# Optimization experiments

Measured on AMD Instinct MI355X. Metric: run time of the kernel, lower is better.

The kernel has to match this reference:

```python
import jax, jax.numpy as jnp
import numpy as np

# Dims (match init_kwargs)
B, S, D = 2, 2048, 2048
H = 16
Q_LORA, KV_LORA = 768, 512
NOPE, ROPE, VD = 128, 64, 128
QHD = NOPE + ROPE  # 192


def setup_inputs() -> dict:
    key = jax.random.key(0)
    ks = jax.random.split(key, 7)
    w = lambda k, shape: (jax.random.normal(k, shape, jnp.float32) * 0.02)
    return {
        "x": jax.random.normal(ks[0], (B, S, D), jnp.float32),
        "position": jnp.broadcast_to(jnp.arange(S, dtype=jnp.int32), (B, S)),
        "mask": jnp.tril(jnp.ones((1, 1, S, S), jnp.int32)),  # causal
        "w_q_down": w(ks[1], (D, Q_LORA)),                 # (in, out) layout
        "w_q_up": w(ks[2], (Q_LORA, H * QHD)),
        "w_kv_down": w(ks[3], (D, KV_LORA + ROPE)),
        "w_kv_up": w(ks[4], (KV_LORA, H * (NOPE + VD))),
        "w_out": w(ks[5], (H * VD, D)),
    }


def reference(x, position, mask, w_q_down, w_q_up, w_kv_down, w_kv_up, w_out):
    # position unused: rope_embedding is None in the source module.
    # Low-rank Q: down then up projection.
    q = (x @ w_q_down) @ w_q_up                      # [B,S,H*QHD]
    q = q.reshape(B, S, H, QHD).transpose(0, 2, 1, 3)  # [B,H,S,QHD]
    q_nope, q_rope = q[..., :NOPE], q[..., NOPE:]

    # Low-rank KV: down projection yields compressed kv + shared rope key.
    c = x @ w_kv_down                                # [B,S,KV_LORA+ROPE]
    c_kv, k_rope = c[..., :KV_LORA], c[..., KV_LORA:]
    k_rope = k_rope[:, None, :, :]                   # [B,1,S,ROPE]

    kv = (c_kv @ w_kv_up).reshape(B, S, H, NOPE + VD).transpose(0, 2, 1, 3)
    k_nope, v = kv[..., :NOPE], kv[..., NOPE:]       # [B,H,S,NOPE], [B,H,S,VD]

    q_state = jnp.concatenate([q_nope, q_rope], axis=-1)           # [B,H,S,QHD]
    k_state = jnp.concatenate(
        [k_nope, jnp.broadcast_to(k_rope, (B, H, S, ROPE))], axis=-1)

    scale = 1.0 / jnp.sqrt(jnp.float32(VD))  # source divides by sqrt(v_head_dim)
    scores = jnp.einsum("bhqd,bhkd->bhqk", q_state, k_state) * scale
    scores = jnp.where(mask == 0, jnp.float32(-jnp.inf), scores)
    att = jax.nn.softmax(scores, axis=-1)            # dropout_rate=0 (eval)
    out = jnp.einsum("bhqk,bhkd->bhqd", att, v)      # [B,H,S,VD]
    out = out.transpose(0, 2, 1, 3).reshape(B, S, H * VD)
    return out @ w_out
```

## Files before the change

kernel.cpp:

```cpp
#include <hip/hip_runtime.h>

typedef __bf16 bf16;
typedef bf16 bf16x8 __attribute__((ext_vector_type(8)));
typedef bf16 bf16x4 __attribute__((ext_vector_type(4)));
typedef float f32x4 __attribute__((ext_vector_type(4)));
typedef short s16x4 __attribute__((ext_vector_type(4)));

#define AS1 __attribute__((address_space(1)))
#define AS3 __attribute__((address_space(3)))

__device__ __forceinline__ void load_lds16(const void* g, void* l) {
    __builtin_amdgcn_global_load_lds((const AS1 unsigned int*)g,
                                     (AS3 unsigned int*)l, 16, 0, 0);
}

__global__ __launch_bounds__(256) void cast_f32_bf16(
        const float* __restrict__ in, bf16* __restrict__ out, int n) {
    int i = (blockIdx.x * 256 + threadIdx.x) * 4;
    if (i < n) {
        float4 v = *(const float4*)(in + i);
        bf16x4 o = { (bf16)v.x, (bf16)v.y, (bf16)v.z, (bf16)v.w };
        *(bf16x4*)(out + i) = o;
    }
}

__global__ __launch_bounds__(256) void transpose_cast(
        const float* __restrict__ in, bf16* __restrict__ out,
        int K, int N, int Np) {
    __shared__ float tile[32][33];
    int bx = blockIdx.x * 32;
    int by = blockIdx.y * 32;
    int tx = threadIdx.x, ty = threadIdx.y;
#pragma unroll
    for (int i = 0; i < 4; ++i) {
        int k = by + ty + i * 8, n = bx + tx;
        float v = (k < K && n < N) ? in[(size_t)k * N + n] : 0.f;
        tile[ty + i * 8][tx] = v;
    }
    __syncthreads();
#pragma unroll
    for (int i = 0; i < 4; ++i) {
        int n = bx + ty + i * 8, k = by + tx;
        if (n < Np && k < K) out[(size_t)n * K + k] = (bf16)tile[tx][ty + i * 8];
    }
}

template <typename OutT>
__global__ __launch_bounds__(256) void gemm_bt(
        const bf16* __restrict__ A, const bf16* __restrict__ Bt,
        OutT* __restrict__ C, int K, int lda, int ldb, int ldc) {
    __shared__ __align__(16) bf16 As[128 * 64];
    __shared__ __align__(16) bf16 Bs[128 * 64];
    const int tid = threadIdx.x;
    const int wave = tid >> 6, lane = tid & 63;
    const int l15 = lane & 15, quad = lane >> 4;
    const int m0 = blockIdx.y * 128, n0 = blockIdx.x * 128;
    const int wm = (wave >> 1) * 64, wn = (wave & 1) * 64;

    f32x4 acc[4][4] = {};

    for (int k0 = 0; k0 < K; k0 += 64) {
#pragma unroll
        for (int c = 0; c < 4; ++c) {
            int e = wave * 2048 + c * 512 + lane * 8;
            int r = e >> 6, col = e & 63;
            load_lds16(A + (size_t)(m0 + r) * lda + k0 + col,
                       &As[wave * 2048 + c * 512]);
            load_lds16(Bt + (size_t)(n0 + r) * ldb + k0 + col,
                       &Bs[wave * 2048 + c * 512]);
        }
        __syncthreads();
#pragma unroll
        for (int kk = 0; kk < 64; kk += 32) {
            bf16x8 af[4], bf[4];
#pragma unroll
            for (int i = 0; i < 4; ++i)
                af[i] = *(const bf16x8*)&As[(wm + i * 16 + l15) * 64 + kk + quad * 8];
#pragma unroll
            for (int j = 0; j < 4; ++j)
                bf[j] = *(const bf16x8*)&Bs[(wn + j * 16 + l15) * 64 + kk + quad * 8];
#pragma unroll
            for (int i = 0; i < 4; ++i)
#pragma unroll
                for (int j = 0; j < 4; ++j)
                    acc[i][j] = __builtin_amdgcn_mfma_f32_16x16x32_bf16(
                        af[i], bf[j], acc[i][j], 0, 0, 0);
        }
        __syncthreads();
    }
#pragma unroll
    for (int i = 0; i < 4; ++i)
#pragma unroll
        for (int j = 0; j < 4; ++j) {
            int row = m0 + wm + i * 16 + quad * 4;
            int col = n0 + wn + j * 16 + l15;
#pragma unroll
            for (int r = 0; r < 4; ++r)
                C[(size_t)(row + r) * ldc + col] = (OutT)acc[i][j][r];
        }
}

__global__ __launch_bounds__(256) void gemm_down(
        const bf16* __restrict__ A, const bf16* __restrict__ Bt,
        bf16* __restrict__ C1, bf16* __restrict__ C2) {
    const int K = 2048, lda = 2048, ldb = 2048;
    __shared__ __align__(16) bf16 As[128 * 64];
    __shared__ __align__(16) bf16 Bs[128 * 64];
    const int tid = threadIdx.x;
    const int wave = tid >> 6, lane = tid & 63;
    const int l15 = lane & 15, quad = lane >> 4;
    const int m0 = blockIdx.y * 128, n0 = blockIdx.x * 128;
    const int wm = (wave >> 1) * 64, wn = (wave & 1) * 64;

    f32x4 acc[4][4] = {};

    for (int k0 = 0; k0 < K; k0 += 64) {
#pragma unroll
        for (int c = 0; c < 4; ++c) {
            int e = wave * 2048 + c * 512 + lane * 8;
            int r = e >> 6, col = e & 63;
            load_lds16(A + (size_t)(m0 + r) * lda + k0 + col,
                       &As[wave * 2048 + c * 512]);
            load_lds16(Bt + (size_t)(n0 + r) * ldb + k0 + col,
                       &Bs[wave * 2048 + c * 512]);
        }
        __syncthreads();
#pragma unroll
        for (int kk = 0; kk < 64; kk += 32) {
            bf16x8 af[4], bf[4];
#pragma unroll
            for (int i = 0; i < 4; ++i)
                af[i] = *(const bf16x8*)&As[(wm + i * 16 + l15) * 64 + kk + quad * 8];
#pragma unroll
            for (int j = 0; j < 4; ++j)
                bf[j] = *(const bf16x8*)&Bs[(wn + j * 16 + l15) * 64 + kk + quad * 8];
#pragma unroll
            for (int i = 0; i < 4; ++i)
#pragma unroll
                for (int j = 0; j < 4; ++j)
                    acc[i][j] = __builtin_amdgcn_mfma_f32_16x16x32_bf16(
                        af[i], bf[j], acc[i][j], 0, 0, 0);
        }
        __syncthreads();
    }
    bf16* Cp; int ldc, coff;
    if (n0 < 768) { Cp = C1; ldc = 768; coff = 0; }
    else          { Cp = C2; ldc = 640; coff = 768; }
#pragma unroll
    for (int i = 0; i < 4; ++i)
#pragma unroll
        for (int j = 0; j < 4; ++j) {
            int row = m0 + wm + i * 16 + quad * 4;
            int col = n0 + wn + j * 16 + l15 - coff;
#pragma unroll
            for (int r = 0; r < 4; ++r)
                Cp[(size_t)(row + r) * ldc + col] = (bf16)acc[i][j][r];
        }
}

__global__ __launch_bounds__(512) void mla_attention(
        const bf16* __restrict__ qb, const bf16* __restrict__ kvb,
        const bf16* __restrict__ cb, bf16* __restrict__ ob) {
    constexpr int S = 2048;
    const int qt = gridDim.x - 1 - blockIdx.x;
    const int h = blockIdx.y, b = blockIdx.z;
    const int q0 = qt * 128;
    const int tid = threadIdx.x, wave = tid >> 6, lane = tid & 63;
    const int l15 = lane & 15, quad = lane >> 4;

    __shared__ __align__(16) bf16 Ks[24 * 512];
    __shared__ __align__(16) bf16 Vt[128 * 68];

    const int qrow = q0 + wave * 16 + l15;
    bf16x8 qf[6];
    {
        const bf16* qr = qb + (size_t)(b * S + qrow) * 3072 + h * 192;
#pragma unroll
        for (int ks = 0; ks < 6; ++ks)
            qf[ks] = *(const bf16x8*)(qr + ks * 32 + quad * 8);
    }

    f32x4 o[8] = {};
    float m_i = -1e30f, l_i = 0.f;
    const float sm_scale = 0.08838834764831845f * 1.4426950408889634f;

    const int ntiles = 2 * qt + 2;
    const int qmax_w = q0 + wave * 16 + 15;

    bf16x8 vreg[2];
    {
        const bf16* vr = kvb + (size_t)(b * S + lane) * 4096 + h * 256 + 128 + wave * 16;
        vreg[0] = *(const bf16x8*)(vr);
        vreg[1] = *(const bf16x8*)(vr + 8);
    }

    for (int kt = 0; kt < ntiles; ++kt) {
        const int kv0 = kt * 64;
        __syncthreads();
#pragma unroll
        for (int i = 0; i < 3; ++i) {
            const int bi = wave * 3 + i;
            const int mt = bi / 6, ks = bi % 6;
            const size_t row = (size_t)(b * S + kv0 + mt * 16 + l15);
            const bf16* g = (ks < 4)
                ? kvb + row * 4096 + h * 256 + ks * 32 + quad * 8
                : cb  + row * 640  + 512 + (ks - 4) * 32 + quad * 8;
            load_lds16(g, &Ks[bi * 512]);
        }
#pragma unroll
        for (int c = 0; c < 2; ++c)
#pragma unroll
            for (int u = 0; u < 8; ++u)
                Vt[(wave * 16 + c * 8 + u) * 68 + lane] = vreg[c][u];
        __syncthreads();

        if (kt + 1 < ntiles) {
            const bf16* vr = kvb + (size_t)(b * S + (kt + 1) * 64 + lane) * 4096
                             + h * 256 + 128 + wave * 16;
            vreg[0] = *(const bf16x8*)(vr);
            vreg[1] = *(const bf16x8*)(vr + 8);
        }

        if (kv0 > qmax_w) continue;

        f32x4 s[4];
#pragma unroll
        for (int mt = 0; mt < 4; ++mt) {
            f32x4 a = {};
#pragma unroll
            for (int ks = 0; ks < 6; ++ks) {
                bf16x8 kf = *(const bf16x8*)&Ks[(mt * 6 + ks) * 512 + lane * 8];
                a = __builtin_amdgcn_mfma_f32_16x16x32_bf16(kf, qf[ks], a, 0, 0, 0);
            }
            s[mt] = a;
        }

        float mx = -1e30f;
#pragma unroll
        for (int mt = 0; mt < 4; ++mt)
#pragma unroll
            for (int r = 0; r < 4; ++r) {
                int kvi = kv0 + mt * 16 + quad * 4 + r;
                float v = (kvi <= qrow) ? s[mt][r] * sm_scale : -1e30f;
                s[mt][r] = v;
                mx = fmaxf(mx, v);
            }
        mx = fmaxf(mx, __shfl_xor(mx, 16, 64));
        mx = fmaxf(mx, __shfl_xor(mx, 32, 64));
        float m_new = fmaxf(m_i, mx);
        float su = 0.f;
        bf16x4 pf[4];
#pragma unroll
        for (int mt = 0; mt < 4; ++mt)
#pragma unroll
            for (int r = 0; r < 4; ++r) {
                float p = exp2f(s[mt][r] - m_new);
                su += p;
                pf[mt][r] = (bf16)p;
            }
        su += __shfl_xor(su, 16, 64);
        su += __shfl_xor(su, 32, 64);
        float alpha = exp2f(m_i - m_new);
        l_i = l_i * alpha + su;
        m_i = m_new;
        float alpha_r[4];
#pragma unroll
        for (int r = 0; r < 4; ++r) alpha_r[r] = __shfl(alpha, quad * 4 + r, 64);
#pragma unroll
        for (int nt = 0; nt < 8; ++nt)
#pragma unroll
            for (int r = 0; r < 4; ++r) o[nt][r] *= alpha_r[r];

#pragma unroll
        for (int ktk = 0; ktk < 4; ++ktk) {
            s16x4 a = __builtin_bit_cast(s16x4, pf[ktk]);
#pragma unroll
            for (int nt = 0; nt < 8; ++nt) {
                s16x4 bfv = __builtin_bit_cast(s16x4,
                    *(const bf16x4*)&Vt[(nt * 16 + l15) * 68 + ktk * 16 + quad * 4]);
                o[nt] = __builtin_amdgcn_mfma_f32_16x16x16bf16_1k(a, bfv, o[nt], 0, 0, 0);
            }
        }
    }

    float l_r[4];
#pragma unroll
    for (int r = 0; r < 4; ++r) l_r[r] = __shfl(l_i, quad * 4 + r, 64);
    bf16* obase = ob + (size_t)(b * S + q0 + wave * 16) * 2048 + h * 128;
#pragma unroll
    for (int nt = 0; nt < 8; ++nt)
#pragma unroll
        for (int r = 0; r < 4; ++r)
            obase[(size_t)(quad * 4 + r) * 2048 + nt * 16 + l15] =
                (bf16)(o[nt][r] / l_r[r]);
}

extern "C" void kernel_launch(void* const* d_in, const int* in_sizes, int n_in,
                              void* d_out, int out_size, void* d_ws, size_t ws_size,
                              hipStream_t stream) {
    const float* x    = (const float*)d_in[0];
    const float* wqd  = (const float*)d_in[3];
    const float* wqu  = (const float*)d_in[4];
    const float* wkvd = (const float*)d_in[5];
    const float* wkvu = (const float*)d_in[6];
    const float* wout = (const float*)d_in[7];
    float* out = (float*)d_out;
    char* ws = (char*)d_ws;

    bf16* xb    = (bf16*)(ws + 0);
    bf16* wqdT  = (bf16*)(ws + 16777216);
    bf16* wkvdT = (bf16*)(ws + 19922944);
    bf16* wquT  = (bf16*)(ws + 22544384);
    bf16* wkvuT = (bf16*)(ws + 27262976);
    bf16* woutT = (bf16*)(ws + 31457280);
    bf16* qd    = (bf16*)(ws + 39845888);
    bf16* qb    = (bf16*)(ws + 46137344);
    bf16* cb    = (bf16*)(ws + 71303168);
    bf16* kvb   = (bf16*)(ws + 76546048);
    bf16* attnb = (bf16*)(ws + 110100480);

    dim3 tb(32, 8);
    cast_f32_bf16<<<8192, 256, 0, stream>>>(x, xb, 8388608);
    transpose_cast<<<dim3(24, 64),  tb, 0, stream>>>(wqd,  wqdT,  2048, 768,  768);
    transpose_cast<<<dim3(20, 64),  tb, 0, stream>>>(wkvd, wkvdT, 2048, 576,  640);
    transpose_cast<<<dim3(96, 24),  tb, 0, stream>>>(wqu,  wquT,  768,  3072, 3072);
    transpose_cast<<<dim3(128, 16), tb, 0, stream>>>(wkvu, wkvuT, 512,  4096, 4096);
    transpose_cast<<<dim3(64, 64),  tb, 0, stream>>>(wout, woutT, 2048, 2048, 2048);

    gemm_down<<<dim3(11, 32), 256, 0, stream>>>(xb, wqdT, qd, cb);
    gemm_bt<bf16><<<dim3(24, 32), 256, 0, stream>>>(qd, wquT,  qb,  768, 768, 768, 3072);
    gemm_bt<bf16><<<dim3(32, 32), 256, 0, stream>>>(cb, wkvuT, kvb, 512, 640, 512, 4096);

    mla_attention<<<dim3(16, 16, 2), 512, 0, stream>>>(qb, kvb, cb, attnb);

    gemm_bt<float><<<dim3(16, 32), 256, 0, stream>>>(attnb, woutT, out, 2048, 2048, 2048, 2048);
}
```

Before: 510.2 us.

## Pre-transpose V and double-buffer K/V tiles via async LDS loads in attention

Adds a separate kernel that writes V transposed per head into the workspace, reusing the x buffer once x is no longer needed. The attention kernel then loads both K and V tiles into double-buffered LDS with direct global-to-LDS loads, prefetching the next tile while computing the current one. This replaces the register-staged V transpose and removes one barrier per tile. It also skips mask evaluation on tiles that lie fully below the diagonal. The cost is an extra kernel launch, an extra pass over V in memory, and twice the LDS footprint, which may reduce occupancy.

```diff
diff --git a/kernel.cpp b/kernel.cpp
--- a/kernel.cpp
+++ b/kernel.cpp
@@ -43,6 +43,25 @@
         int n = bx + ty + i * 8, k = by + tx;
         if (n < Np && k < K) out[(size_t)n * K + k] = (bf16)tile[tx][ty + i * 8];
     }
+}
+
+__global__ __launch_bounds__(256) void transpose_v(
+        const bf16* __restrict__ kvb, bf16* __restrict__ vtb) {
+    __shared__ bf16 t[32][34];
+    const int kv0 = blockIdx.x * 32;
+    const int vd0 = blockIdx.y * 32;
+    const int bh = blockIdx.z;
+    const int b = bh >> 4, h = bh & 15;
+    const int tx = threadIdx.x, ty = threadIdx.y;
+#pragma unroll
+    for (int i = 0; i < 4; ++i)
+        t[ty + i * 8][tx] = kvb[(size_t)(b * 2048 + kv0 + ty + i * 8) * 4096
+                                + h * 256 + 128 + vd0 + tx];
+    __syncthreads();
+#pragma unroll
+    for (int i = 0; i < 4; ++i)
+        vtb[(size_t)(bh * 128 + vd0 + ty + i * 8) * 2048 + kv0 + tx] =
+            t[tx][ty + i * 8];
 }
 
 template <typename OutT>
@@ -160,7 +179,8 @@
 
 __global__ __launch_bounds__(512) void mla_attention(
         const bf16* __restrict__ qb, const bf16* __restrict__ kvb,
-        const bf16* __restrict__ cb, bf16* __restrict__ ob) {
+        const bf16* __restrict__ cb, const bf16* __restrict__ vtb,
+        bf16* __restrict__ ob) {
     constexpr int S = 2048;
     const int qt = gridDim.x - 1 - blockIdx.x;
     const int h = blockIdx.y, b = blockIdx.z;
@@ -168,8 +188,8 @@
     const int tid = threadIdx.x, wave = tid >> 6, lane = tid & 63;
     const int l15 = lane & 15, quad = lane >> 4;
 
-    __shared__ __align__(16) bf16 Ks[24 * 512];
-    __shared__ __align__(16) bf16 Vt[128 * 68];
+    __shared__ __align__(16) bf16 Ks[2][24 * 512];
+    __shared__ __align__(16) bf16 Vs[2][8 * 1024];
 
     const int qrow = q0 + wave * 16 + l15;
     bf16x8 qf[6];
@@ -180,23 +200,9 @@
             qf[ks] = *(const bf16x8*)(qr + ks * 32 + quad * 8);
     }
 
-    f32x4 o[8] = {};
-    float m_i = -1e30f, l_i = 0.f;
-    const float sm_scale = 0.08838834764831845f * 1.4426950408889634f;
-
-    const int ntiles = 2 * qt + 2;
-    const int qmax_w = q0 + wave * 16 + 15;
-
-    bf16x8 vreg[2];
-    {
-        const bf16* vr = kvb + (size_t)(b * S + lane) * 4096 + h * 256 + 128 + wave * 16;
-        vreg[0] = *(const bf16x8*)(vr);
-        vreg[1] = *(const bf16x8*)(vr + 8);
-    }
-
-    for (int kt = 0; kt < ntiles; ++kt) {
-        const int kv0 = kt * 64;
-        __syncthreads();
+    const bf16* vt_head = vtb + (size_t)((b * 16 + h) * 128) * 2048;
+
+    auto stage = [&](int kv0, int p) {
 #pragma unroll
         for (int i = 0; i < 3; ++i) {
             const int bi = wave * 3 + i;
@@ -205,21 +211,30 @@
             const bf16* g = (ks < 4)
                 ? kvb + row * 4096 + h * 256 + ks * 32 + quad * 8
                 : cb  + row * 640  + 512 + (ks - 4) * 32 + quad * 8;
-            load_lds16(g, &Ks[bi * 512]);
-        }
-#pragma unroll
-        for (int c = 0; c < 2; ++c)
-#pragma unroll
-            for (int u = 0; u < 8; ++u)
-                Vt[(wave * 16 + c * 8 + u) * 68 + lane] = vreg[c][u];
-        __syncthreads();
-
-        if (kt + 1 < ntiles) {
-            const bf16* vr = kvb + (size_t)(b * S + (kt + 1) * 64 + lane) * 4096
-                             + h * 256 + 128 + wave * 16;
-            vreg[0] = *(const bf16x8*)(vr);
-            vreg[1] = *(const bf16x8*)(vr + 8);
-        }
+            load_lds16(g, &Ks[p][bi * 512]);
+        }
+#pragma unroll
+        for (int i = 0; i < 2; ++i) {
+            const bf16* g = vt_head + (size_t)(wave * 16 + l15) * 2048
+                            + kv0 + (i * 4 + quad) * 8;
+            load_lds16(g, &Vs[p][wave * 1024 + i * 512]);
+        }
+    };
+
+    f32x4 o[8] = {};
+    float m_i = -1e30f, l_i = 0.f;
+    const float sm_scale = 0.08838834764831845f * 1.4426950408889634f;
+    const int ntiles = 2 * qt + 2;
+    const int qmin_w = q0 + wave * 16;
+    const int qmax_w = qmin_w + 15;
+
+    stage(0, 0);
+
+    for (int kt = 0; kt < ntiles; ++kt) {
+        const int kv0 = kt * 64;
+        const int p = kt & 1;
+        __syncthreads();
+        if (kt + 1 < ntiles) stage(kv0 + 64, p ^ 1);
 
         if (kv0 > qmax_w) continue;
 
@@ -229,22 +244,33 @@
             f32x4 a = {};
 #pragma unroll
             for (int ks = 0; ks < 6; ++ks) {
-                bf16x8 kf = *(const bf16x8*)&Ks[(mt * 6 + ks) * 512 + lane * 8];
+                bf16x8 kf = *(const bf16x8*)&Ks[p][(mt * 6 + ks) * 512 + lane * 8];
                 a = __builtin_amdgcn_mfma_f32_16x16x32_bf16(kf, qf[ks], a, 0, 0, 0);
             }
             s[mt] = a;
         }
 
         float mx = -1e30f;
-#pragma unroll
-        for (int mt = 0; mt < 4; ++mt)
-#pragma unroll
-            for (int r = 0; r < 4; ++r) {
-                int kvi = kv0 + mt * 16 + quad * 4 + r;
-                float v = (kvi <= qrow) ? s[mt][r] * sm_scale : -1e30f;
-                s[mt][r] = v;
-                mx = fmaxf(mx, v);
-            }
+        if (kv0 + 63 > qmin_w) {
+#pragma unroll
+            for (int mt = 0; mt < 4; ++mt)
+#pragma unroll
+                for (int r = 0; r < 4; ++r) {
+                    int kvi = kv0 + mt * 16 + quad * 4 + r;
+                    float v = (kvi <= qrow) ? s[mt][r] * sm_scale : -1e30f;
+                    s[mt][r] = v;
+                    mx = fmaxf(mx, v);
+                }
+        } else {
+#pragma unroll
+            for (int mt = 0; mt < 4; ++mt)
+#pragma unroll
+                for (int r = 0; r < 4; ++r) {
+                    float v = s[mt][r] * sm_scale;
+                    s[mt][r] = v;
+                    mx = fmaxf(mx, v);
+                }
+        }
         mx = fmaxf(mx, __shfl_xor(mx, 16, 64));
         mx = fmaxf(mx, __shfl_xor(mx, 32, 64));
         float m_new = fmaxf(m_i, mx);
@@ -254,9 +280,9 @@
         for (int mt = 0; mt < 4; ++mt)
 #pragma unroll
             for (int r = 0; r < 4; ++r) {
-                float p = exp2f(s[mt][r] - m_new);
-                su += p;
-                pf[mt][r] = (bf16)p;
+                float pv = exp2f(s[mt][r] - m_new);
+                su += pv;
+                pf[mt][r] = (bf16)pv;
             }
         su += __shfl_xor(su, 16, 64);
         su += __shfl_xor(su, 32, 64);
@@ -274,10 +300,11 @@
 #pragma unroll
         for (int ktk = 0; ktk < 4; ++ktk) {
             s16x4 a = __builtin_bit_cast(s16x4, pf[ktk]);
+            const int voff = ktk * 256 + (quad >> 1) * 128 + l15 * 8 + (quad & 1) * 4;
 #pragma unroll
             for (int nt = 0; nt < 8; ++nt) {
                 s16x4 bfv = __builtin_bit_cast(s16x4,
-                    *(const bf16x4*)&Vt[(nt * 16 + l15) * 68 + ktk * 16 + quad * 4]);
+                    *(const bf16x4*)&Vs[p][nt * 1024 + voff]);
                 o[nt] = __builtin_amdgcn_mfma_f32_16x16x16bf16_1k(a, bfv, o[nt], 0, 0, 0);
             }
         }
@@ -308,6 +335,7 @@
     char* ws = (char*)d_ws;
 
     bf16* xb    = (bf16*)(ws + 0);
+    bf16* vtb   = (bf16*)(ws + 0);
     bf16* wqdT  = (bf16*)(ws + 16777216);
     bf16* wkvdT = (bf16*)(ws + 19922944);
     bf16* wquT  = (bf16*)(ws + 22544384);
@@ -331,7 +359,9 @@
     gemm_bt<bf16><<<dim3(24, 32), 256, 0, stream>>>(qd, wquT,  qb,  768, 768, 768, 3072);
     gemm_bt<bf16><<<dim3(32, 32), 256, 0, stream>>>(cb, wkvuT, kvb, 512, 640, 512, 4096);
 
-    mla_attention<<<dim3(16, 16, 2), 512, 0, stream>>>(qb, kvb, cb, attnb);
+    transpose_v<<<dim3(64, 4, 32), tb, 0, stream>>>(kvb, vtb);
+
+    mla_attention<<<dim3(16, 16, 2), 512, 0, stream>>>(qb, kvb, cb, vtb, attnb);
 
     gemm_bt<float><<<dim3(16, 32), 256, 0, stream>>>(attnb, woutT, out, 2048, 2048, 2048, 2048);
 }
```

After: 546.0 us. 1.07x slower.
